# Performance work log

Measured on AMD Instinct MI355X. Metric: run time of the kernel, lower is better.

Reference implementation:

```python
import jax, jax.numpy as jnp
import numpy as np

B = 4096
ED = 128          # EMBEDDING_DIM
HD = 64           # HIDDEN_DIM
LH = 128          # LSTM_HIDDEN_DIM
IN_DIM = ED * (12 + 48 + 1)  # 7808
N_ABILITY, N_MOVE = 300, 900


def setup_inputs() -> dict:
    key = jax.random.key(0)
    ks = jax.random.split(key, 16)
    s = lambda k, shape, scale=0.05: (jax.random.normal(k, shape, dtype=jnp.float32) * scale)
    return {
        "ability_ids": jax.random.randint(ks[0], (B, 12), 0, N_ABILITY),
        "move_ids": jax.random.randint(ks[1], (B, 48), 0, N_MOVE),
        "numerical": s(ks[2], (B, 84), 1.0),
        "mask": (jax.random.uniform(ks[3], (B, 9)) > 0.3).astype(jnp.float32),
        "h0": jnp.zeros((B, LH), jnp.float32),
        "c0": jnp.zeros((B, LH), jnp.float32),
        "ability_emb": s(ks[4], (N_ABILITY, ED), 1.0),
        "move_emb": s(ks[5], (N_MOVE, ED), 1.0),
        "num_W": s(ks[6], (ED, 84)),
        "num_b": s(ks[7], (ED,)),
        "Wih": s(ks[8], (4 * LH, IN_DIM), 0.01),
        "Whh": s(ks[9], (4 * LH, LH)),
        "bih": s(ks[10], (4 * LH,)),
        "bhh": s(ks[11], (4 * LH,)),
        "W1": s(ks[12], (HD, LH)),
        "b1": s(ks[13], (HD,)),
        "W2": s(ks[14], (ED, HD)),
        "b2": s(ks[15], (ED,)),
        "Wa": s(jax.random.fold_in(key, 100), (9, ED)),
        "ba": s(jax.random.fold_in(key, 101), (9,)),
    }


def reference(ability_ids, move_ids, numerical, mask, h0, c0,
              ability_emb, move_emb, num_W, num_b,
              Wih, Whh, bih, bhh, W1, b1, W2, b2, Wa, ba):
    # Gather + concat: [B, 12*ED] + [B, 48*ED] + [B, ED] -> [B, 7808]
    ab = ability_emb[ability_ids].reshape(ability_ids.shape[0], 12 * ED)
    mv = move_emb[move_ids].reshape(move_ids.shape[0], 48 * ED)
    num = numerical @ num_W.T + num_b
    x = jnp.concatenate([ab, mv, num], axis=-1)

    # Single-timestep LSTM (torch gate order: i, f, g, o)
    gates = x @ Wih.T + bih + h0 @ Whh.T + bhh
    i, f, g, o = jnp.split(gates, 4, axis=-1)
    i, f, o = jax.nn.sigmoid(i), jax.nn.sigmoid(f), jax.nn.sigmoid(o)
    g = jnp.tanh(g)
    c1 = f * c0 + i * g
    h1 = o * jnp.tanh(c1)

    # MLP head + action logits
    feat = jax.nn.relu(h1 @ W1.T + b1) @ W2.T + b2
    probs = jax.nn.softmax(feat @ Wa.T + ba, axis=-1)

    # Masked renormalization; fall back to unmasked probs when mask kills everything
    masked = probs * mask
    ssum = masked.sum(-1, keepdims=True)
    out = jnp.where(ssum > 0, masked / jnp.where(ssum > 0, ssum, 1.0), probs)
    return out, h1, c1
```

## Files before the change

### kernel.cpp

```cpp
#include <hip/hip_runtime.h>
#include <hip/hip_bf16.h>
#include <stdint.h>
#include <stddef.h>

typedef __bf16 bf16;
typedef __bf16 bf16x8 __attribute__((ext_vector_type(8)));
typedef float f32x4 __attribute__((ext_vector_type(4)));

#define BATCH 4096
#define KIH 7808
#define KTOT 7936
#define NG 512
#define LH 128
#define HD 64
#define ED 128
#define SPLITK 4

#define OFF_WCAT 0u
#define OFF_GPART 8126464u
#define OFF_XT   41680896u
#define OFF_AB   43778048u
#define OFF_MV   43854848u
#define OFF_ADDR 44085248u
#define OFF_H1B  46182400u
#define OFF_W1F  47230976u
#define OFF_W2F  47247360u
#define OFF_WAF  47263744u

#define O_H1 (BATCH * 9)
#define O_C1 (BATCH * 9 + BATCH * LH)

typedef const __attribute__((address_space(1))) uint32_t* gas_ptr;
typedef __attribute__((address_space(3))) uint32_t* las_ptr;

__device__ __forceinline__ void async16(const void* g, void* l) {
    __builtin_amdgcn_global_load_lds((gas_ptr)g, (las_ptr)l, 16, 0, 0);
}

__global__ void prep(const int* __restrict__ ab_ids,
                     const int* __restrict__ mv_ids,
                     const float* __restrict__ numerical,
                     const float* __restrict__ h0,
                     const float* __restrict__ numW,
                     const float* __restrict__ numb,
                     const float* __restrict__ Wih,
                     const float* __restrict__ Whh,
                     const float* __restrict__ ab_emb,
                     const float* __restrict__ mv_emb,
                     const float* __restrict__ W1,
                     const float* __restrict__ W2,
                     const float* __restrict__ Wa,
                     uint8_t* __restrict__ ws) {
    const int bid = blockIdx.x;
    const int t = threadIdx.x;

    if (bid < BATCH) {
        bf16* xtail = (bf16*)(ws + OFF_XT);
        uint32_t* addrs = (uint32_t*)(ws + OFF_ADDR);
        const int b = bid;

        __shared__ int ids[60];
        __shared__ float numr[84];
        if (t < 60) ids[t] = (t < 12) ? ab_ids[b * 12 + t] : mv_ids[b * 48 + (t - 12)];
        if (t >= 128 && t < 128 + 84) numr[t - 128] = numerical[(size_t)b * 84 + (t - 128)];
        __syncthreads();

        if (t < 128) {
            float acc = numb[t];
#pragma unroll 4
            for (int k = 0; k < 84; ++k)
                acc += numr[k] * numW[t * 84 + k];
            xtail[(size_t)b * 256 + t] = (bf16)acc;
        } else {
            const int tt = t - 128;
            xtail[(size_t)b * 256 + 128 + tt] = (bf16)h0[(size_t)b * LH + tt];
        }

        if (t < 64) {
            uint32_t off;
            if (t < 12) off = OFF_AB + (uint32_t)ids[t] * 256u;
            else if (t < 60) off = OFF_MV + (uint32_t)ids[t] * 256u;
            else if (t == 60) off = OFF_XT + (uint32_t)b * 512u;
            else if (t == 61) off = OFF_XT + (uint32_t)b * 512u + 256u;
            else off = OFF_XT;
            addrs[(size_t)b * 64 + t] = off;
        }
    } else if (bid < BATCH + 512) {
        bf16* Wcat = (bf16*)(ws + OFF_WCAT);
        const int n = bid - BATCH;
        const float* src_ih = Wih + (size_t)n * KIH;
        const float* src_hh = Whh + (size_t)n * LH;
        bf16* dst = Wcat + (size_t)n * KTOT;
        for (int k4 = t; k4 < KTOT / 4; k4 += 256) {
            const int k = k4 * 4;
            const float4 v = (k < KIH) ? *(const float4*)(src_ih + k)
                                       : *(const float4*)(src_hh + (k - KIH));
            bf16 o0 = (bf16)v.x, o1 = (bf16)v.y, o2 = (bf16)v.z, o3 = (bf16)v.w;
            dst[k] = o0; dst[k + 1] = o1; dst[k + 2] = o2; dst[k + 3] = o3;
        }
    } else if (bid < BATCH + 512 + 600) {
        bf16* ab8 = (bf16*)(ws + OFF_AB);
        bf16* mv8 = (bf16*)(ws + OFF_MV);
        const int i = (bid - BATCH - 512) * 256 + t;
        if (i < 300 * 128) ab8[i] = (bf16)ab_emb[i];
        else if (i < 1200 * 128) mv8[i - 300 * 128] = (bf16)mv_emb[i - 300 * 128];
    } else {
        bf16* W1f = (bf16*)(ws + OFF_W1F);
        bf16* W2f = (bf16*)(ws + OFF_W2F);
        bf16* Waf = (bf16*)(ws + OFF_WAF);
        for (int e = t; e < 8192; e += 256) {
            const int j = e & 7, ln = (e >> 3) & 63, fid = e >> 9;
            const int kt = fid & 3, nt = fid >> 2;
            const int n = nt * 16 + (ln & 15);
            const int k = kt * 32 + (ln >> 4) * 8 + j;
            W1f[e] = (bf16)W1[n * 128 + k];
        }
        for (int e = t; e < 8192; e += 256) {
            const int j = e & 7, ln = (e >> 3) & 63, fid = e >> 9;
            const int kt = fid & 1, nt = fid >> 1;
            const int n = nt * 16 + (ln & 15);
            const int k = kt * 32 + (ln >> 4) * 8 + j;
            W2f[e] = (bf16)W2[n * 64 + k];
        }
        for (int e = t; e < 2048; e += 256) {
            const int j = e & 7, ln = (e >> 3) & 63, kt = e >> 9;
            const int n = ln & 15;
            const int k = kt * 32 + (ln >> 4) * 8 + j;
            Waf[e] = (n < 9) ? (bf16)Wa[n * 128 + k] : (bf16)0.f;
        }
    }
}

__global__ __launch_bounds__(256, 2) void gemm_gates(
    const uint8_t* __restrict__ wsbase,
    const bf16* __restrict__ Wcat,
    const uint32_t* __restrict__ addrs,
    float* __restrict__ gpart) {
    __shared__ bf16 As[2][128 * 64];
    __shared__ bf16 Bs[2][128 * 64];
    __shared__ uint32_t adr[17][128];

    const int tid = threadIdx.x;
    const int w = tid >> 6;
    const int lane = tid & 63;
    const int bm = blockIdx.x;
    const int bn = blockIdx.y;
    const int bz = blockIdx.z;
    const int kt_beg = bz * 31;
    const int kt_end = kt_beg + 31;

    const int s0 = kt_beg >> 1;
    const int ns = ((kt_end - 1) >> 1) - s0 + 1;
    for (int i = tid; i < ns * 128; i += 256) {
        adr[i >> 7][i & 127] =
            addrs[(size_t)(bm * 128 + (i & 127)) * 64 + s0 + (i >> 7)];
    }

    const int r_l = lane >> 3;
    const int sc16 = ((lane & 7) ^ r_l) * 16;

    const int wn = w & 1;
    const int wk = w >> 1;
    const int n0 = wn * 64;
    const int kk8 = wk * 4 + (lane >> 4);
    const int fl = lane & 15;

    f32x4 acc[8][4];
#pragma unroll
    for (int i = 0; i < 8; ++i)
#pragma unroll
        for (int j = 0; j < 4; ++j)
#pragma unroll
            for (int r = 0; r < 4; ++r) acc[i][j][r] = 0.f;

    __syncthreads();

    auto stage = [&](int kt, int pb) {
        const int k0 = kt * 64;
        const int sl = (kt >> 1) - s0;
        const int hb = (kt & 1) * 128;
#pragma unroll
        for (int j = 0; j < 4; ++j) {
            const int row = (w * 4 + j) * 8 + r_l;
            const uint8_t* gsrc = wsbase + adr[sl][row] + hb + sc16;
            async16(gsrc, (void*)&As[pb][((w * 4 + j) * 64 + lane) * 8]);
        }
#pragma unroll
        for (int j = 0; j < 4; ++j) {
            const int row = (w * 4 + j) * 8 + r_l;
            const bf16* gsrc = Wcat + (size_t)(bn * 128 + row) * KTOT + k0 + (sc16 >> 1);
            async16(gsrc, (void*)&Bs[pb][((w * 4 + j) * 64 + lane) * 8]);
        }
    };

    stage(kt_beg, 0);

    for (int kt = kt_beg; kt < kt_end; ++kt) {
        const int pb = (kt - kt_beg) & 1;
        __syncthreads();
        if (kt + 1 < kt_end) stage(kt + 1, pb ^ 1);

        const bf16* Ab = &As[pb][0];
        const bf16* Bb = &Bs[pb][0];

        bf16x8 bfr[4];
#pragma unroll
        for (int tj = 0; tj < 4; ++tj) {
            const int n = n0 + tj * 16 + fl;
            bfr[tj] = *(const bf16x8*)&Bb[n * 64 + ((kk8 ^ (n & 7)) * 8)];
        }
#pragma unroll
        for (int ti = 0; ti < 8; ++ti) {
            const int m = ti * 16 + fl;
            const bf16x8 af = *(const bf16x8*)&Ab[m * 64 + ((kk8 ^ (m & 7)) * 8)];
#pragma unroll
            for (int tj = 0; tj < 4; ++tj)
                acc[ti][tj] = __builtin_amdgcn_mfma_f32_16x16x32_bf16(
                    af, bfr[tj], acc[ti][tj], 0, 0, 0);
        }
    }

    __syncthreads();
    float* red = (wn == 0) ? (float*)&As[0][0] : (float*)&Bs[0][0];
    if (wk == 1) {
#pragma unroll
        for (int ti = 0; ti < 8; ++ti)
#pragma unroll
            for (int tj = 0; tj < 4; ++tj)
#pragma unroll
                for (int r = 0; r < 4; ++r)
                    red[((ti * 4 + tj) * 4 + r) * 64 + lane] = acc[ti][tj][r];
    }
    __syncthreads();

    if (wk == 0) {
        float* gdst = gpart + (size_t)bz * BATCH * NG;
        const int mlo = (lane >> 4) * 4;
#pragma unroll
        for (int ti = 0; ti < 8; ++ti)
#pragma unroll
            for (int tj = 0; tj < 4; ++tj) {
                const int mg = bm * 128 + ti * 16 + mlo;
                const int ng = bn * 128 + n0 + tj * 16 + fl;
                float* dst = gdst + (size_t)mg * NG + ng;
#pragma unroll
                for (int r = 0; r < 4; ++r)
                    dst[(size_t)r * NG] =
                        acc[ti][tj][r] + red[((ti * 4 + tj) * 4 + r) * 64 + lane];
            }
    }
}

__global__ void reduce_lstm(const float* __restrict__ gpart,
                            const float* __restrict__ bih,
                            const float* __restrict__ bhh,
                            const float* __restrict__ c0,
                            float* __restrict__ out,
                            bf16* __restrict__ h1b) {
    const int t = threadIdx.x;
    const int b = blockIdx.x * 2 + (t >> 7);
    const int u = t & 127;

    float gv[4];
#pragma unroll
    for (int q = 0; q < 4; ++q)
        gv[q] = bih[q * 128 + u] + bhh[q * 128 + u];
#pragma unroll
    for (int z = 0; z < SPLITK; ++z) {
        const float* gz = gpart + ((size_t)z * BATCH + b) * NG + u;
#pragma unroll
        for (int q = 0; q < 4; ++q) gv[q] += gz[q * 128];
    }

    const float iv = 1.f / (1.f + __expf(-gv[0]));
    const float fv = 1.f / (1.f + __expf(-gv[1]));
    const float gg = tanhf(gv[2]);
    const float ov = 1.f / (1.f + __expf(-gv[3]));
    const float c1 = fv * c0[(size_t)b * LH + u] + iv * gg;
    const float h1 = ov * tanhf(c1);

    out[O_H1 + (size_t)b * LH + u] = h1;
    out[O_C1 + (size_t)b * LH + u] = c1;
    h1b[(size_t)b * LH + u] = (bf16)h1;
}

__global__ __launch_bounds__(64) void mlp_head(
    const bf16* __restrict__ h1b, const float* __restrict__ mask,
    const bf16* __restrict__ W1f, const bf16* __restrict__ W2f,
    const bf16* __restrict__ Waf,
    const float* __restrict__ b1, const float* __restrict__ b2,
    const float* __restrict__ ba,
    float* __restrict__ out) {
    __shared__ bf16 uS[16 * 64];
    __shared__ bf16 fS[16 * 128];

    const int lane = threadIdx.x;
    const int b0 = blockIdx.x * 16;
    const int nl = lane & 15, kg = lane >> 4;

    bf16x8 ah[4];
#pragma unroll
    for (int kt = 0; kt < 4; ++kt)
        ah[kt] = *(const bf16x8*)&h1b[(size_t)(b0 + nl) * 128 + kt * 32 + kg * 8];

#pragma unroll
    for (int nt = 0; nt < 4; ++nt) {
        f32x4 a = {0.f, 0.f, 0.f, 0.f};
#pragma unroll
        for (int kt = 0; kt < 4; ++kt)
            a = __builtin_amdgcn_mfma_f32_16x16x32_bf16(
                ah[kt], *(const bf16x8*)&W1f[((nt * 4 + kt) * 64 + lane) * 8],
                a, 0, 0, 0);
        const int n = nt * 16 + nl;
        const float bb = b1[n];
#pragma unroll
        for (int r = 0; r < 4; ++r)
            uS[(kg * 4 + r) * 64 + n] = (bf16)fmaxf(a[r] + bb, 0.f);
    }
    __syncthreads();

    bf16x8 au[2];
#pragma unroll
    for (int kt = 0; kt < 2; ++kt)
        au[kt] = *(const bf16x8*)&uS[nl * 64 + kt * 32 + kg * 8];

#pragma unroll
    for (int nt = 0; nt < 8; ++nt) {
        f32x4 a = {0.f, 0.f, 0.f, 0.f};
#pragma unroll
        for (int kt = 0; kt < 2; ++kt)
            a = __builtin_amdgcn_mfma_f32_16x16x32_bf16(
                au[kt], *(const bf16x8*)&W2f[((nt * 2 + kt) * 64 + lane) * 8],
                a, 0, 0, 0);
        const int n = nt * 16 + nl;
        const float bb = b2[n];
#pragma unroll
        for (int r = 0; r < 4; ++r)
            fS[(kg * 4 + r) * 128 + n] = (bf16)(a[r] + bb);
    }
    __syncthreads();

    bf16x8 afr[4];
#pragma unroll
    for (int kt = 0; kt < 4; ++kt)
        afr[kt] = *(const bf16x8*)&fS[nl * 128 + kt * 32 + kg * 8];

    f32x4 lg4 = {0.f, 0.f, 0.f, 0.f};
#pragma unroll
    for (int kt = 0; kt < 4; ++kt)
        lg4 = __builtin_amdgcn_mfma_f32_16x16x32_bf16(
            afr[kt], *(const bf16x8*)&Waf[(kt * 64 + lane) * 8], lg4, 0, 0, 0);

    const float bav = (nl < 9) ? ba[nl] : 0.f;

#pragma unroll
    for (int r = 0; r < 4; ++r) {
        const int b = b0 + kg * 4 + r;
        float lg = (nl < 9) ? lg4[r] + bav : -1e30f;
        float mx = lg;
#pragma unroll
        for (int off = 1; off < 16; off <<= 1)
            mx = fmaxf(mx, __shfl_xor(mx, off, 64));
        const float e = (nl < 9) ? __expf(lg - mx) : 0.f;
        const float mv = (nl < 9) ? mask[(size_t)b * 9 + nl] : 0.f;
        float tot = e, ms = e * mv;
#pragma unroll
        for (int off = 1; off < 16; off <<= 1) {
            tot += __shfl_xor(tot, off, 64);
            ms += __shfl_xor(ms, off, 64);
        }
        if (nl < 9)
            out[(size_t)b * 9 + nl] = (ms > 0.f) ? e * mv / ms : e / tot;
    }
}

extern "C" void kernel_launch(void* const* d_in, const int* in_sizes, int n_in,
                              void* d_out, int out_size, void* d_ws, size_t ws_size,
                              hipStream_t stream) {
    const int* ab_ids = (const int*)d_in[0];
    const int* mv_ids = (const int*)d_in[1];
    const float* numerical = (const float*)d_in[2];
    const float* mask = (const float*)d_in[3];
    const float* h0 = (const float*)d_in[4];
    const float* c0 = (const float*)d_in[5];
    const float* ab_emb = (const float*)d_in[6];
    const float* mv_emb = (const float*)d_in[7];
    const float* numW = (const float*)d_in[8];
    const float* numb = (const float*)d_in[9];
    const float* Wih = (const float*)d_in[10];
    const float* Whh = (const float*)d_in[11];
    const float* bih = (const float*)d_in[12];
    const float* bhh = (const float*)d_in[13];
    const float* W1 = (const float*)d_in[14];
    const float* b1 = (const float*)d_in[15];
    const float* W2 = (const float*)d_in[16];
    const float* b2 = (const float*)d_in[17];
    const float* Wa = (const float*)d_in[18];
    const float* ba = (const float*)d_in[19];
    float* out = (float*)d_out;

    uint8_t* ws = (uint8_t*)d_ws;
    bf16* Wcat = (bf16*)(ws + OFF_WCAT);
    float* gpart = (float*)(ws + OFF_GPART);
    uint32_t* addrs = (uint32_t*)(ws + OFF_ADDR);
    bf16* h1b = (bf16*)(ws + OFF_H1B);
    bf16* W1f = (bf16*)(ws + OFF_W1F);
    bf16* W2f = (bf16*)(ws + OFF_W2F);
    bf16* Waf = (bf16*)(ws + OFF_WAF);

    prep<<<BATCH + 512 + 600 + 1, 256, 0, stream>>>(
        ab_ids, mv_ids, numerical, h0, numW, numb, Wih, Whh, ab_emb, mv_emb,
        W1, W2, Wa, ws);
    gemm_gates<<<dim3(32, 4, SPLITK), 256, 0, stream>>>(ws, Wcat, addrs, gpart);
    reduce_lstm<<<BATCH / 2, 256, 0, stream>>>(gpart, bih, bhh, c0, out, h1b);
    mlp_head<<<BATCH / 16, 64, 0, stream>>>(h1b, mask, W1f, W2f, Waf,
                                            b1, b2, ba, out);
}
```

Measured before the change: 181.0 us.

## Fold numerical projection into Wih and store split-K partials as bf16

Instead of computing numerical@num_W^T per batch row in prep, the last 128 columns of Wih are pre-multiplied by num_W, so the GEMM consumes raw numerical features padded to 128. The num_b contribution becomes a per-gate bias added in reduce_lstm. Split-K partial gate sums are also written and read as bf16 instead of fp32, halving that intermediate traffic. This removes per-row matvec work and reduces workspace bandwidth, but adds rounding error from bf16 partials and the folded weights.

```diff
diff --git a/kernel.cpp b/kernel.cpp
--- a/kernel.cpp
+++ b/kernel.cpp
@@ -18,14 +18,15 @@
 
 #define OFF_WCAT 0u
 #define OFF_GPART 8126464u
-#define OFF_XT   41680896u
-#define OFF_AB   43778048u
-#define OFF_MV   43854848u
-#define OFF_ADDR 44085248u
-#define OFF_H1B  46182400u
-#define OFF_W1F  47230976u
-#define OFF_W2F  47247360u
-#define OFF_WAF  47263744u
+#define OFF_XT   24903680u
+#define OFF_AB   27000832u
+#define OFF_MV   27077632u
+#define OFF_ADDR 27308032u
+#define OFF_H1B  28356608u
+#define OFF_W1F  29405184u
+#define OFF_W2F  29421568u
+#define OFF_WAF  29437952u
+#define OFF_NB   29442048u
 
 #define O_H1 (BATCH * 9)
 #define O_C1 (BATCH * 9 + BATCH * LH)
@@ -60,21 +61,16 @@
         const int b = bid;
 
         __shared__ int ids[60];
-        __shared__ float numr[84];
         if (t < 60) ids[t] = (t < 12) ? ab_ids[b * 12 + t] : mv_ids[b * 48 + (t - 12)];
-        if (t >= 128 && t < 128 + 84) numr[t - 128] = numerical[(size_t)b * 84 + (t - 128)];
-        __syncthreads();
 
         if (t < 128) {
-            float acc = numb[t];
-#pragma unroll 4
-            for (int k = 0; k < 84; ++k)
-                acc += numr[k] * numW[t * 84 + k];
-            xtail[(size_t)b * 256 + t] = (bf16)acc;
+            const float v = (t < 84) ? numerical[(size_t)b * 84 + t] : 0.f;
+            xtail[(size_t)b * 256 + t] = (bf16)v;
         } else {
             const int tt = t - 128;
             xtail[(size_t)b * 256 + 128 + tt] = (bf16)h0[(size_t)b * LH + tt];
         }
+        __syncthreads();
 
         if (t < 64) {
             uint32_t off;
@@ -87,16 +83,40 @@
         }
     } else if (bid < BATCH + 512) {
         bf16* Wcat = (bf16*)(ws + OFF_WCAT);
+        float* nbias = (float*)(ws + OFF_NB);
         const int n = bid - BATCH;
+
+        __shared__ float wrow[128];
+        __shared__ float nbs[128];
+        if (t < 128) wrow[t] = Wih[(size_t)n * KIH + 7680 + t];
+        else nbs[t - 128] = numb[t - 128];
+        __syncthreads();
+
         const float* src_ih = Wih + (size_t)n * KIH;
-        const float* src_hh = Whh + (size_t)n * LH;
         bf16* dst = Wcat + (size_t)n * KTOT;
-        for (int k4 = t; k4 < KTOT / 4; k4 += 256) {
+        for (int k4 = t; k4 < 1920; k4 += 256) {
             const int k = k4 * 4;
-            const float4 v = (k < KIH) ? *(const float4*)(src_ih + k)
-                                       : *(const float4*)(src_hh + (k - KIH));
+            const float4 v = *(const float4*)(src_ih + k);
             bf16 o0 = (bf16)v.x, o1 = (bf16)v.y, o2 = (bf16)v.z, o3 = (bf16)v.w;
             dst[k] = o0; dst[k + 1] = o1; dst[k + 2] = o2; dst[k + 3] = o3;
+        }
+        if (t < 84) {
+            float acc = 0.f;
+#pragma unroll 4
+            for (int e = 0; e < 128; ++e)
+                acc += wrow[e] * numW[e * 84 + t];
+            dst[7680 + t] = (bf16)acc;
+        } else if (t < 128) {
+            dst[7680 + t] = (bf16)0.f;
+        } else {
+            const int tt = t - 128;
+            dst[KIH + tt] = (bf16)Whh[(size_t)n * LH + tt];
+        }
+        if (t == 255) {
+            float a = 0.f;
+#pragma unroll 4
+            for (int e = 0; e < 128; ++e) a += wrow[e] * nbs[e];
+            nbias[n] = a;
         }
     } else if (bid < BATCH + 512 + 600) {
         bf16* ab8 = (bf16*)(ws + OFF_AB);
@@ -135,7 +155,7 @@
     const uint8_t* __restrict__ wsbase,
     const bf16* __restrict__ Wcat,
     const uint32_t* __restrict__ addrs,
-    float* __restrict__ gpart) {
+    bf16* __restrict__ gpart) {
     __shared__ bf16 As[2][128 * 64];
     __shared__ bf16 Bs[2][128 * 64];
     __shared__ uint32_t adr[17][128];
@@ -234,7 +254,7 @@
     __syncthreads();
 
     if (wk == 0) {
-        float* gdst = gpart + (size_t)bz * BATCH * NG;
+        bf16* gdst = gpart + (size_t)bz * BATCH * NG;
         const int mlo = (lane >> 4) * 4;
 #pragma unroll
         for (int ti = 0; ti < 8; ++ti)
@@ -242,18 +262,19 @@
             for (int tj = 0; tj < 4; ++tj) {
                 const int mg = bm * 128 + ti * 16 + mlo;
                 const int ng = bn * 128 + n0 + tj * 16 + fl;
-                float* dst = gdst + (size_t)mg * NG + ng;
+                bf16* dst = gdst + (size_t)mg * NG + ng;
 #pragma unroll
                 for (int r = 0; r < 4; ++r)
-                    dst[(size_t)r * NG] =
-                        acc[ti][tj][r] + red[((ti * 4 + tj) * 4 + r) * 64 + lane];
+                    dst[(size_t)r * NG] = (bf16)(
+                        acc[ti][tj][r] + red[((ti * 4 + tj) * 4 + r) * 64 + lane]);
             }
     }
 }
 
-__global__ void reduce_lstm(const float* __restrict__ gpart,
+__global__ void reduce_lstm(const bf16* __restrict__ gpart,
                             const float* __restrict__ bih,
                             const float* __restrict__ bhh,
+                            const float* __restrict__ nbias,
                             const float* __restrict__ c0,
                             float* __restrict__ out,
                             bf16* __restrict__ h1b) {
@@ -264,12 +285,12 @@
     float gv[4];
 #pragma unroll
     for (int q = 0; q < 4; ++q)
-        gv[q] = bih[q * 128 + u] + bhh[q * 128 + u];
+        gv[q] = bih[q * 128 + u] + bhh[q * 128 + u] + nbias[q * 128 + u];
 #pragma unroll
     for (int z = 0; z < SPLITK; ++z) {
-        const float* gz = gpart + ((size_t)z * BATCH + b) * NG + u;
-#pragma unroll
-        for (int q = 0; q < 4; ++q) gv[q] += gz[q * 128];
+        const bf16* gz = gpart + ((size_t)z * BATCH + b) * NG + u;
+#pragma unroll
+        for (int q = 0; q < 4; ++q) gv[q] += (float)gz[q * 128];
     }
 
     const float iv = 1.f / (1.f + __expf(-gv[0]));
@@ -401,18 +422,20 @@
 
     uint8_t* ws = (uint8_t*)d_ws;
     bf16* Wcat = (bf16*)(ws + OFF_WCAT);
-    float* gpart = (float*)(ws + OFF_GPART);
+    bf16* gpart = (bf16*)(ws + OFF_GPART);
     uint32_t* addrs = (uint32_t*)(ws + OFF_ADDR);
     bf16* h1b = (bf16*)(ws + OFF_H1B);
     bf16* W1f = (bf16*)(ws + OFF_W1F);
     bf16* W2f = (bf16*)(ws + OFF_W2F);
     bf16* Waf = (bf16*)(ws + OFF_WAF);
+    float* nbias = (float*)(ws + OFF_NB);
 
     prep<<<BATCH + 512 + 600 + 1, 256, 0, stream>>>(
         ab_ids, mv_ids, numerical, h0, numW, numb, Wih, Whh, ab_emb, mv_emb,
         W1, W2, Wa, ws);
     gemm_gates<<<dim3(32, 4, SPLITK), 256, 0, stream>>>(ws, Wcat, addrs, gpart);
-    reduce_lstm<<<BATCH / 2, 256, 0, stream>>>(gpart, bih, bhh, c0, out, h1b);
+    reduce_lstm<<<BATCH / 2, 256, 0, stream>>>(gpart, bih, bhh, nbias, c0,
+                                               out, h1b);
     mlp_head<<<BATCH / 16, 64, 0, stream>>>(h1b, mask, W1f, W2f, Waf,
                                             b1, b2, ba, out);
 }
```

New measurement: 171.4 us. 5.3% less time.
